# Kernel tuning notes

Measured on AMD Instinct MI355X. Metric: run time of the kernel, lower is better.

The kernel has to match this reference:

```python
import jax, jax.numpy as jnp
import numpy as np


def setup_inputs() -> dict:
    key = jax.random.key(0)
    k1, k2, k3 = jax.random.split(key, 3)
    B, H, S, D = 2, 16, 2048, 64
    q = jax.random.normal(k1, (B, H, S, D), dtype=jnp.float32)
    k = jax.random.normal(k2, (B, H, S, D), dtype=jnp.float32)
    v = jax.random.normal(k3, (B, H, S, D), dtype=jnp.float32)
    return {"q": q, "k": k, "v": v}


def reference(q, k, v):
    # q,k,v: [B,H,S,D]; causal attention with 1/sqrt(D) scaling, fp32 softmax.
    scale = 1.0 / (q.shape[-1] ** 0.5)
    scores = jnp.einsum('bhqd,bhkd->bhqk', q * scale, k)  # [B,H,S,S]
    S = scores.shape[-1]
    causal_mask = jnp.triu(jnp.ones((S, S), dtype=bool), k=1)
    scores = jnp.where(causal_mask, -jnp.inf, scores)
    attn = jax.nn.softmax(scores.astype(jnp.float32), axis=-1).astype(q.dtype)
    output = jnp.einsum('bhqk,bhkd->bhqd', attn, v)
    # Module also returns an all-zeros attn_weights placeholder of shape [B,H,S,S]
    attn_weights = jnp.zeros(scores.shape, dtype=q.dtype)
    return (output, attn_weights)
```

## Files before the change

### kernel.cpp

```cpp
#include <hip/hip_runtime.h>


typedef __bf16 bf16x8 __attribute__((ext_vector_type(8)));
typedef float f32x4 __attribute__((ext_vector_type(4)));

#define LOG2E 1.44269504088896340736f

__device__ __forceinline__ unsigned short f2bf(float f) {
  unsigned int u = __float_as_uint(f);
  u += 0x7fffu + ((u >> 16) & 1u);
  return (unsigned short)(u >> 16);
}

constexpr int Sdim = 2048, Ddim = 64, BHn = 32;
constexpr int QTiles = 32;
constexpr int LDK = 72;
constexpr int OUT0 = BHn * Sdim * Ddim;

__device__ __forceinline__ int vswz_m(int d) { return ((d >> 2) ^ (d >> 5)) & 7; }

__global__ __launch_bounds__(256, 3)
void flash_causal_kernel(const float* __restrict__ Q, const float* __restrict__ K,
                         const float* __restrict__ V, float* __restrict__ out) {
  __shared__ unsigned short Klds[2][64 * LDK];
  __shared__ unsigned short Vlds[2][64 * LDK];
  __shared__ unsigned short Plds[4][16 * LDK];

  const int tid  = threadIdx.x;
  const int wave = tid >> 6;
  const int lane = tid & 63;
  const int quad = lane >> 4;
  const int l15  = lane & 15;

  const int bh = blockIdx.x & (BHn - 1);
  const int g  = (int)(blockIdx.x >> 5);
  const int qt = (g & 1) ? (QTiles - 1 - (g >> 1)) : (g >> 1);

  const int base  = bh * Sdim * Ddim;
  const int qrow0 = qt * 64 + wave * 16;

  bf16x8 aq[2];
  {
    const float* qp = Q + base + (qrow0 + l15) * Ddim + quad * 8;
    #pragma unroll
    for (int s = 0; s < 2; ++s) {
      float4 a = *(const float4*)(qp + 32 * s);
      float4 b = *(const float4*)(qp + 32 * s + 4);
      union { unsigned short u[8]; bf16x8 v; } u;
      u.u[0] = f2bf(a.x * 0.125f); u.u[1] = f2bf(a.y * 0.125f);
      u.u[2] = f2bf(a.z * 0.125f); u.u[3] = f2bf(a.w * 0.125f);
      u.u[4] = f2bf(b.x * 0.125f); u.u[5] = f2bf(b.y * 0.125f);
      u.u[6] = f2bf(b.z * 0.125f); u.u[7] = f2bf(b.w * 0.125f);
      aq[s] = u.v;
    }
  }

  f32x4 ot[4];
  #pragma unroll
  for (int t = 0; t < 4; ++t) ot[t] = (f32x4){0.f, 0.f, 0.f, 0.f};
  float mrun = -__builtin_inff(), lrun = 0.f;

  const float4* kg4 = (const float4*)(K + base);
  const float4* vg4 = (const float4*)(V + base);

  float4 kf[4], vf[4];

  auto stage = [&](int buf) {
    #pragma unroll
    for (int i = 0; i < 4; ++i) {
      int lin = i * 256 + tid;
      int row = lin >> 4;
      int c4  = (lin & 15) << 2;
      uint2 t2;
      t2.x = (unsigned int)f2bf(kf[i].x) | ((unsigned int)f2bf(kf[i].y) << 16);
      t2.y = (unsigned int)f2bf(kf[i].z) | ((unsigned int)f2bf(kf[i].w) << 16);
      *(uint2*)&Klds[buf][row * LDK + c4] = t2;
      const int sw = vswz_m(c4) << 3;
      Vlds[buf][(c4 + 0) * LDK + (row ^ sw)] = f2bf(vf[i].x);
      Vlds[buf][(c4 + 1) * LDK + (row ^ sw)] = f2bf(vf[i].y);
      Vlds[buf][(c4 + 2) * LDK + (row ^ sw)] = f2bf(vf[i].z);
      Vlds[buf][(c4 + 3) * LDK + (row ^ sw)] = f2bf(vf[i].w);
    }
  };

  #pragma unroll
  for (int i = 0; i < 4; ++i) { kf[i] = kg4[i * 256 + tid]; vf[i] = vg4[i * 256 + tid]; }
  stage(0);
  if (qt >= 1) {
    const float4* kp = kg4 + 1024;
    const float4* vp = vg4 + 1024;
    #pragma unroll
    for (int i = 0; i < 4; ++i) { kf[i] = kp[i * 256 + tid]; vf[i] = vp[i * 256 + tid]; }
  }

  for (int j = 0; j <= qt; ++j) {
    __syncthreads();
    if (j < qt) stage((j + 1) & 1);
    if (j + 2 <= qt) {
      const float4* kp = kg4 + (j + 2) * 1024;
      const float4* vp = vg4 + (j + 2) * 1024;
      #pragma unroll
      for (int i = 0; i < 4; ++i) { kf[i] = kp[i * 256 + tid]; vf[i] = vp[i * 256 + tid]; }
    }

    const unsigned short* Kb = Klds[j & 1];
    const unsigned short* Vb = Vlds[j & 1];

    f32x4 sc[4];
    #pragma unroll
    for (int t = 0; t < 4; ++t) sc[t] = (f32x4){0.f, 0.f, 0.f, 0.f};
    #pragma unroll
    for (int s = 0; s < 2; ++s) {
      #pragma unroll
      for (int t = 0; t < 4; ++t) {
        bf16x8 ka = *(const bf16x8*)&Kb[(16 * t + l15) * LDK + 32 * s + quad * 8];
        sc[t] = __builtin_amdgcn_mfma_f32_16x16x32_bf16(ka, aq[s], sc[t], 0, 0, 0);
      }
    }

    if (j == qt) {
      const int qml = wave * 16 + l15;
      #pragma unroll
      for (int t = 0; t < 4; ++t)
        #pragma unroll
        for (int r = 0; r < 4; ++r)
          if (16 * t + 4 * quad + r > qml) sc[t][r] = -__builtin_inff();
    }

    float mx = sc[0][0];
    #pragma unroll
    for (int t = 0; t < 4; ++t)
      #pragma unroll
      for (int r = 0; r < 4; ++r) mx = fmaxf(mx, sc[t][r]);
    mx = fmaxf(mx, __shfl_xor(mx, 16));
    mx = fmaxf(mx, __shfl_xor(mx, 32));
    float mn    = fmaxf(mrun, mx);
    float alpha = __builtin_amdgcn_exp2f((mrun - mn) * LOG2E);
    float msc   = mn * LOG2E;
    mrun = mn;
    float rs = 0.f;
    #pragma unroll
    for (int t = 0; t < 4; ++t)
      #pragma unroll
      for (int r = 0; r < 4; ++r) {
        float p = __builtin_amdgcn_exp2f(fmaf(sc[t][r], LOG2E, -msc));
        sc[t][r] = p;
        rs += p;
      }
    rs += __shfl_xor(rs, 16);
    rs += __shfl_xor(rs, 32);
    lrun = lrun * alpha + rs;
    #pragma unroll
    for (int t = 0; t < 4; ++t)
      #pragma unroll
      for (int r = 0; r < 4; ++r) ot[t][r] *= alpha;

    #pragma unroll
    for (int t = 0; t < 4; ++t) {
      uint2 pw;
      pw.x = (unsigned int)f2bf(sc[t][0]) | ((unsigned int)f2bf(sc[t][1]) << 16);
      pw.y = (unsigned int)f2bf(sc[t][2]) | ((unsigned int)f2bf(sc[t][3]) << 16);
      *(uint2*)&Plds[wave][l15 * LDK + 16 * t + 4 * quad] = pw;
    }

    #pragma unroll
    for (int s = 0; s < 2; ++s) {
      bf16x8 pb = *(const bf16x8*)&Plds[wave][l15 * LDK + 32 * s + quad * 8];
      #pragma unroll
      for (int t = 0; t < 4; ++t) {
        const int d = 16 * t + l15;
        const int knb = ((4 * s + quad) ^ vswz_m(d)) << 3;
        bf16x8 va = *(const bf16x8*)&Vb[d * LDK + knb];
        ot[t] = __builtin_amdgcn_mfma_f32_16x16x32_bf16(va, pb, ot[t], 0, 0, 0);
      }
    }
  }

  {
    float inv = 1.0f / lrun;
    float* orow = out + base + (qrow0 + l15) * Ddim + 4 * quad;
    #pragma unroll
    for (int t = 0; t < 4; ++t) {
      f32x4 o4;
      o4.x = ot[t][0] * inv; o4.y = ot[t][1] * inv;
      o4.z = ot[t][2] * inv; o4.w = ot[t][3] * inv;
      *(f32x4*)(orow + 16 * t) = o4;
    }
  }

  {
    const int gp = (QTiles - 1) - qt;
    const int w  = 2 * gp + 1;
    const size_t start_f4 = (size_t)1024 * (32 * (size_t)(gp * gp) + (size_t)bh * w);
    const size_t count_f4 = (size_t)1024 * w;
    f32x4 z4 = (f32x4){0.f, 0.f, 0.f, 0.f};
    f32x4* zp = (f32x4*)(out + OUT0) + start_f4;
    for (size_t i = tid; i < count_f4; i += 256)
      __builtin_nontemporal_store(z4, zp + i);
  }
}

extern "C" void kernel_launch(void* const* d_in, const int* in_sizes, int n_in,
                              void* d_out, int out_size, void* d_ws, size_t ws_size,
                              hipStream_t stream) {
  const float* q = (const float*)d_in[0];
  const float* k = (const float*)d_in[1];
  const float* v = (const float*)d_in[2];
  float* out = (float*)d_out;
  dim3 grid(BHn * QTiles);
  flash_causal_kernel<<<grid, dim3(256), 0, stream>>>(q, k, v, out);
}
```

Baseline: 598.1 us.

## Process two query tiles per block to share staged K/V tiles

Each workgroup now computes 128 query rows as two 64-row fragments, reusing each bf16-staged K/V tile in LDS for both fragments' QK and PV MFMAs. This halves global K/V loads and conversion/staging work per query row, and the grid shrinks accordingly. The zero-fill of the attention-weights placeholder is re-partitioned per head across the new blocks. Register pressure roughly doubles for accumulators, so launch bounds drop to 2 blocks per CU, reducing occupancy and latency hiding.

Result: no change. 586.6 us (-1.9%).

```diff
diff --git a/kernel.cpp b/kernel.cpp
--- a/kernel.cpp
+++ b/kernel.cpp
@@ -13,18 +13,19 @@
 }
 
 constexpr int Sdim = 2048, Ddim = 64, BHn = 32;
-constexpr int QTiles = 32;
+constexpr int STiles = 16;
 constexpr int LDK = 72;
 constexpr int OUT0 = BHn * Sdim * Ddim;
+constexpr size_t FILL_PER_BH = 1048576;
 
 __device__ __forceinline__ int vswz_m(int d) { return ((d >> 2) ^ (d >> 5)) & 7; }
 
-__global__ __launch_bounds__(256, 3)
+__global__ __launch_bounds__(256, 2)
 void flash_causal_kernel(const float* __restrict__ Q, const float* __restrict__ K,
                          const float* __restrict__ V, float* __restrict__ out) {
   __shared__ unsigned short Klds[2][64 * LDK];
   __shared__ unsigned short Vlds[2][64 * LDK];
-  __shared__ unsigned short Plds[4][16 * LDK];
+  __shared__ unsigned short Plds[4][2][16 * LDK];
 
   const int tid  = threadIdx.x;
   const int wave = tid >> 6;
@@ -34,37 +35,47 @@
 
   const int bh = blockIdx.x & (BHn - 1);
   const int g  = (int)(blockIdx.x >> 5);
-  const int qt = (g & 1) ? (QTiles - 1 - (g >> 1)) : (g >> 1);
+  const int s  = (g & 1) ? (STiles - 1) - (g >> 1) : (g >> 1);
+  const int jmax = 2 * s + 1;
 
   const int base  = bh * Sdim * Ddim;
-  const int qrow0 = qt * 64 + wave * 16;
-
-  bf16x8 aq[2];
-  {
-    const float* qp = Q + base + (qrow0 + l15) * Ddim + quad * 8;
-    #pragma unroll
-    for (int s = 0; s < 2; ++s) {
-      float4 a = *(const float4*)(qp + 32 * s);
-      float4 b = *(const float4*)(qp + 32 * s + 4);
+  const int qbase = s * 128;
+
+  bf16x8 aq[2][2];
+  #pragma unroll
+  for (int f = 0; f < 2; ++f) {
+    const float* qp = Q + base + (qbase + 64 * f + wave * 16 + l15) * Ddim + quad * 8;
+    #pragma unroll
+    for (int s2 = 0; s2 < 2; ++s2) {
+      float4 a = *(const float4*)(qp + 32 * s2);
+      float4 b = *(const float4*)(qp + 32 * s2 + 4);
       union { unsigned short u[8]; bf16x8 v; } u;
       u.u[0] = f2bf(a.x * 0.125f); u.u[1] = f2bf(a.y * 0.125f);
       u.u[2] = f2bf(a.z * 0.125f); u.u[3] = f2bf(a.w * 0.125f);
       u.u[4] = f2bf(b.x * 0.125f); u.u[5] = f2bf(b.y * 0.125f);
       u.u[6] = f2bf(b.z * 0.125f); u.u[7] = f2bf(b.w * 0.125f);
-      aq[s] = u.v;
-    }
-  }
-
-  f32x4 ot[4];
+      aq[f][s2] = u.v;
+    }
+  }
+
+  f32x4 ot[2][4];
   #pragma unroll
-  for (int t = 0; t < 4; ++t) ot[t] = (f32x4){0.f, 0.f, 0.f, 0.f};
-  float mrun = -__builtin_inff(), lrun = 0.f;
+  for (int f = 0; f < 2; ++f)
+    #pragma unroll
+    for (int t = 0; t < 4; ++t) ot[f][t] = (f32x4){0.f, 0.f, 0.f, 0.f};
+  float mrun[2] = {-__builtin_inff(), -__builtin_inff()};
+  float lrun[2] = {0.f, 0.f};
 
   const float4* kg4 = (const float4*)(K + base);
   const float4* vg4 = (const float4*)(V + base);
-
   float4 kf[4], vf[4];
 
+  auto ldtile = [&](int j) {
+    const float4* kp = kg4 + j * 1024;
+    const float4* vp = vg4 + j * 1024;
+    #pragma unroll
+    for (int i = 0; i < 4; ++i) { kf[i] = kp[i * 256 + tid]; vf[i] = vp[i * 256 + tid]; }
+  };
   auto stage = [&](int buf) {
     #pragma unroll
     for (int i = 0; i < 4; ++i) {
@@ -83,116 +94,117 @@
     }
   };
 
-  #pragma unroll
-  for (int i = 0; i < 4; ++i) { kf[i] = kg4[i * 256 + tid]; vf[i] = vg4[i * 256 + tid]; }
-  stage(0);
-  if (qt >= 1) {
-    const float4* kp = kg4 + 1024;
-    const float4* vp = vg4 + 1024;
-    #pragma unroll
-    for (int i = 0; i < 4; ++i) { kf[i] = kp[i * 256 + tid]; vf[i] = vp[i * 256 + tid]; }
-  }
-
-  for (int j = 0; j <= qt; ++j) {
+  ldtile(0); stage(0); ldtile(1);
+
+  for (int j = 0; j <= jmax; ++j) {
     __syncthreads();
-    if (j < qt) stage((j + 1) & 1);
-    if (j + 2 <= qt) {
-      const float4* kp = kg4 + (j + 2) * 1024;
-      const float4* vp = vg4 + (j + 2) * 1024;
-      #pragma unroll
-      for (int i = 0; i < 4; ++i) { kf[i] = kp[i * 256 + tid]; vf[i] = vp[i * 256 + tid]; }
-    }
+    if (j < jmax) stage((j + 1) & 1);
+    if (j + 2 <= jmax) ldtile(j + 2);
 
     const unsigned short* Kb = Klds[j & 1];
     const unsigned short* Vb = Vlds[j & 1];
-
-    f32x4 sc[4];
-    #pragma unroll
-    for (int t = 0; t < 4; ++t) sc[t] = (f32x4){0.f, 0.f, 0.f, 0.f};
-    #pragma unroll
-    for (int s = 0; s < 2; ++s) {
+    const bool f0act = (j <= 2 * s);
+
+    f32x4 sc[2][4];
+    #pragma unroll
+    for (int f = 0; f < 2; ++f)
+      #pragma unroll
+      for (int t = 0; t < 4; ++t) sc[f][t] = (f32x4){0.f, 0.f, 0.f, 0.f};
+    #pragma unroll
+    for (int s2 = 0; s2 < 2; ++s2) {
       #pragma unroll
       for (int t = 0; t < 4; ++t) {
-        bf16x8 ka = *(const bf16x8*)&Kb[(16 * t + l15) * LDK + 32 * s + quad * 8];
-        sc[t] = __builtin_amdgcn_mfma_f32_16x16x32_bf16(ka, aq[s], sc[t], 0, 0, 0);
-      }
-    }
-
-    if (j == qt) {
-      const int qml = wave * 16 + l15;
+        bf16x8 ka = *(const bf16x8*)&Kb[(16 * t + l15) * LDK + 32 * s2 + quad * 8];
+        sc[0][t] = __builtin_amdgcn_mfma_f32_16x16x32_bf16(ka, aq[0][s2], sc[0][t], 0, 0, 0);
+        sc[1][t] = __builtin_amdgcn_mfma_f32_16x16x32_bf16(ka, aq[1][s2], sc[1][t], 0, 0, 0);
+      }
+    }
+
+    #pragma unroll
+    for (int f = 0; f < 2; ++f) {
+      if (j == 2 * s + f) {
+        const int qml = wave * 16 + l15;
+        #pragma unroll
+        for (int t = 0; t < 4; ++t)
+          #pragma unroll
+          for (int r = 0; r < 4; ++r)
+            if (16 * t + 4 * quad + r > qml) sc[f][t][r] = -__builtin_inff();
+      }
+    }
+
+    #pragma unroll
+    for (int f = 0; f < 2; ++f) {
+      if (f == 0 && !f0act) continue;
+      float mx = sc[f][0][0];
       #pragma unroll
       for (int t = 0; t < 4; ++t)
         #pragma unroll
-        for (int r = 0; r < 4; ++r)
-          if (16 * t + 4 * quad + r > qml) sc[t][r] = -__builtin_inff();
-    }
-
-    float mx = sc[0][0];
-    #pragma unroll
-    for (int t = 0; t < 4; ++t)
-      #pragma unroll
-      for (int r = 0; r < 4; ++r) mx = fmaxf(mx, sc[t][r]);
-    mx = fmaxf(mx, __shfl_xor(mx, 16));
-    mx = fmaxf(mx, __shfl_xor(mx, 32));
-    float mn    = fmaxf(mrun, mx);
-    float alpha = __builtin_amdgcn_exp2f((mrun - mn) * LOG2E);
-    float msc   = mn * LOG2E;
-    mrun = mn;
-    float rs = 0.f;
-    #pragma unroll
-    for (int t = 0; t < 4; ++t)
-      #pragma unroll
-      for (int r = 0; r < 4; ++r) {
-        float p = __builtin_amdgcn_exp2f(fmaf(sc[t][r], LOG2E, -msc));
-        sc[t][r] = p;
-        rs += p;
-      }
-    rs += __shfl_xor(rs, 16);
-    rs += __shfl_xor(rs, 32);
-    lrun = lrun * alpha + rs;
-    #pragma unroll
-    for (int t = 0; t < 4; ++t)
-      #pragma unroll
-      for (int r = 0; r < 4; ++r) ot[t][r] *= alpha;
-
-    #pragma unroll
-    for (int t = 0; t < 4; ++t) {
-      uint2 pw;
-      pw.x = (unsigned int)f2bf(sc[t][0]) | ((unsigned int)f2bf(sc[t][1]) << 16);
-      pw.y = (unsigned int)f2bf(sc[t][2]) | ((unsigned int)f2bf(sc[t][3]) << 16);
-      *(uint2*)&Plds[wave][l15 * LDK + 16 * t + 4 * quad] = pw;
-    }
-
-    #pragma unroll
-    for (int s = 0; s < 2; ++s) {
-      bf16x8 pb = *(const bf16x8*)&Plds[wave][l15 * LDK + 32 * s + quad * 8];
+        for (int r = 0; r < 4; ++r) mx = fmaxf(mx, sc[f][t][r]);
+      mx = fmaxf(mx, __shfl_xor(mx, 16));
+      mx = fmaxf(mx, __shfl_xor(mx, 32));
+      float mn    = fmaxf(mrun[f], mx);
+      float alpha = __builtin_amdgcn_exp2f((mrun[f] - mn) * LOG2E);
+      float msc   = mn * LOG2E;
+      mrun[f] = mn;
+      float rs = 0.f;
+      #pragma unroll
+      for (int t = 0; t < 4; ++t)
+        #pragma unroll
+        for (int r = 0; r < 4; ++r) {
+          float p = __builtin_amdgcn_exp2f(fmaf(sc[f][t][r], LOG2E, -msc));
+          sc[f][t][r] = p;
+          rs += p;
+        }
+      rs += __shfl_xor(rs, 16);
+      rs += __shfl_xor(rs, 32);
+      lrun[f] = lrun[f] * alpha + rs;
+      #pragma unroll
+      for (int t = 0; t < 4; ++t)
+        #pragma unroll
+        for (int r = 0; r < 4; ++r) ot[f][t][r] *= alpha;
+      #pragma unroll
+      for (int t = 0; t < 4; ++t) {
+        uint2 pw;
+        pw.x = (unsigned int)f2bf(sc[f][t][0]) | ((unsigned int)f2bf(sc[f][t][1]) << 16);
+        pw.y = (unsigned int)f2bf(sc[f][t][2]) | ((unsigned int)f2bf(sc[f][t][3]) << 16);
+        *(uint2*)&Plds[wave][f][l15 * LDK + 16 * t + 4 * quad] = pw;
+      }
+    }
+
+    #pragma unroll
+    for (int s2 = 0; s2 < 2; ++s2) {
+      bf16x8 pb0, pb1;
+      if (f0act) pb0 = *(const bf16x8*)&Plds[wave][0][l15 * LDK + 32 * s2 + quad * 8];
+      pb1 = *(const bf16x8*)&Plds[wave][1][l15 * LDK + 32 * s2 + quad * 8];
       #pragma unroll
       for (int t = 0; t < 4; ++t) {
         const int d = 16 * t + l15;
-        const int knb = ((4 * s + quad) ^ vswz_m(d)) << 3;
-        bf16x8 va = *(const bf16x8*)&Vb[d * LDK + knb];
-        ot[t] = __builtin_amdgcn_mfma_f32_16x16x32_bf16(va, pb, ot[t], 0, 0, 0);
-      }
-    }
-  }
-
-  {
-    float inv = 1.0f / lrun;
-    float* orow = out + base + (qrow0 + l15) * Ddim + 4 * quad;
+        bf16x8 va = *(const bf16x8*)&Vb[d * LDK + (((4 * s2 + quad) ^ vswz_m(d)) << 3)];
+        if (f0act)
+          ot[0][t] = __builtin_amdgcn_mfma_f32_16x16x32_bf16(va, pb0, ot[0][t], 0, 0, 0);
+        ot[1][t] = __builtin_amdgcn_mfma_f32_16x16x32_bf16(va, pb1, ot[1][t], 0, 0, 0);
+      }
+    }
+  }
+
+  #pragma unroll
+  for (int f = 0; f < 2; ++f) {
+    float inv = 1.0f / lrun[f];
+    float* orow = out + base + (qbase + 64 * f + wave * 16 + l15) * Ddim + 4 * quad;
     #pragma unroll
     for (int t = 0; t < 4; ++t) {
       f32x4 o4;
-      o4.x = ot[t][0] * inv; o4.y = ot[t][1] * inv;
-      o4.z = ot[t][2] * inv; o4.w = ot[t][3] * inv;
+      o4.x = ot[f][t][0] * inv; o4.y = ot[f][t][1] * inv;
+      o4.z = ot[f][t][2] * inv; o4.w = ot[f][t][3] * inv;
       *(f32x4*)(orow + 16 * t) = o4;
     }
   }
 
   {
-    const int gp = (QTiles - 1) - qt;
+    const int gp = (STiles - 1) - s;
     const int w  = 2 * gp + 1;
-    const size_t start_f4 = (size_t)1024 * (32 * (size_t)(gp * gp) + (size_t)bh * w);
-    const size_t count_f4 = (size_t)1024 * w;
+    const size_t start_f4 = (size_t)bh * FILL_PER_BH + (size_t)4096 * (gp * gp);
+    const size_t count_f4 = (size_t)4096 * w;
     f32x4 z4 = (f32x4){0.f, 0.f, 0.f, 0.f};
     f32x4* zp = (f32x4*)(out + OUT0) + start_f4;
     for (size_t i = tid; i < count_f4; i += 256)
@@ -207,6 +219,6 @@
   const float* k = (const float*)d_in[1];
   const float* v = (const float*)d_in[2];
   float* out = (float*)d_out;
-  dim3 grid(BHn * QTiles);
+  dim3 grid(BHn * STiles);
   flash_causal_kernel<<<grid, dim3(256), 0, stream>>>(q, k, v, out);
 }
```
